# Optimization experiments

Measured on AMD Instinct MI355X. Metric: run time of the kernel, lower is better.

The kernel has to match this reference:

```python
import jax, jax.numpy as jnp
import numpy as np

N_BINS = 15


def setup_inputs() -> dict:
    key = jax.random.key(0)
    k1, k2 = jax.random.split(key)
    N, C = 500000, 100
    logits = jax.random.normal(k1, (N, C), dtype=jnp.float32)
    labels = jax.random.randint(k2, (N,), 0, C, dtype=jnp.int64)
    return {"logits": logits, "labels": labels}


def _classwise_ece(logits, labels, n_bins=N_BINS):
    # Fused equivalent of the per-class, per-bin double loop.
    # Bins are (lower, upper] with boundaries linspace(0,1,n_bins+1),
    # so bin index = ceil(p * n_bins) - 1; p == 0 falls in NO bin.
    probs = jax.nn.softmax(logits, axis=1)            # [N, C]
    N, C = probs.shape
    valid = probs > 0.0                               # p==0 matched by no (lower, upper] bin
    bin_idx = jnp.clip(jnp.ceil(probs * n_bins).astype(jnp.int32) - 1, 0, n_bins - 1)

    class_ids = jnp.arange(C, dtype=jnp.int32)[None, :]          # [1, C]
    key = (jnp.broadcast_to(class_ids * n_bins, probs.shape) + bin_idx).reshape(-1)  # [N*C]

    w = valid.astype(probs.dtype)
    correct = (labels[:, None] == class_ids).astype(probs.dtype)  # labels_in_class

    num_seg = C * n_bins
    count = jax.ops.segment_sum(w.reshape(-1), key, num_segments=num_seg).reshape(C, n_bins)
    conf_sum = jax.ops.segment_sum((probs * w).reshape(-1), key, num_segments=num_seg).reshape(C, n_bins)
    acc_sum = jax.ops.segment_sum((correct * w).reshape(-1), key, num_segments=num_seg).reshape(C, n_bins)

    # |avg_conf - acc| * prop_in_bin == |conf_sum - acc_sum| / N; empty bins give 0.
    per_class_sce = jnp.sum(jnp.abs(conf_sum - acc_sum), axis=1) / N   # [C]
    sce = jnp.mean(per_class_sce)
    return sce, per_class_sce


def reference(logits, labels):
    return _classwise_ece(logits, labels)
```

## Files before the change

### kernel.cpp

```cpp
#include <hip/hip_runtime.h>
#include <math.h>

#define NCLS 100
#define NBINS 15
#define NSEG (NCLS * NBINS)
#define NTOT (2 * NSEG + NCLS)
#define PSTRIDE 3104
#define RPI 8
#define GMAIN 2048
#define NWAVES (GMAIN * 4)

__device__ __forceinline__ void fadd(float* p, float v) { unsafeAtomicAdd(p, v); }

__device__ __forceinline__ float readlane_f(float x, int l) {
    return __builtin_bit_cast(float, __builtin_amdgcn_readlane(__builtin_bit_cast(int, x), l));
}

template <int CTRL>
__device__ __forceinline__ float dpp_add(float x) {
    int y = __builtin_amdgcn_update_dpp(0, __builtin_bit_cast(int, x),
                                        CTRL, 0xf, 0xf, true);
    return x + __builtin_bit_cast(float, y);
}


#define LOAD_TILE(E0, E1, E2, E3, LAB, TB) do {                               \
    (LAB) = labels[min((TB) + lane, N - 1)];                                  \
    const int _f = ((TB) + h) * NCLS + cqc;                                   \
    (E0) = *(const float4*)(logits + min(_f,            flim));               \
    (E1) = *(const float4*)(logits + min(_f + 2 * NCLS, flim));               \
    (E2) = *(const float4*)(logits + min(_f + 4 * NCLS, flim));               \
    (E3) = *(const float4*)(logits + min(_f + 6 * NCLS, flim));               \
} while (0)

#define EXPMASK(E, SOUT, VM) do {                                             \
    float _ex = __expf((E).x), _ey = __expf((E).y);                           \
    float _ez = __expf((E).z), _ew = __expf((E).w);                           \
    (E).x = (VM) ? _ex : 0.f; (E).y = (VM) ? _ey : 0.f;                       \
    (E).z = (VM) ? _ez : 0.f; (E).w = (VM) ? _ew : 0.f;                       \
    SOUT = ((E).x + (E).y) + ((E).z + (E).w);                                 \
} while (0)

#define CLS_TAIL(EV, J, INV, TH, LABV) do {                                   \
    t##J = fmaf((EV), (INV), t##J);                                           \
    const bool _ch = (EV) > (TH);                                             \
    const bool _lh = (cq + (J)) == (LABV);                                    \
    if (_ch || _lh) {                                                         \
        const float _p = (EV) * (INV);                                        \
        const int _b = min((int)ceilf(_p * 15.f) - 1, NBINS - 1);             \
        if (_ch) fadd(&s_conf[(cq + (J)) * NBINS + _b], _p);                  \
        if (_lh) fadd(&s_acc[(cq + (J)) * NBINS + max(_b, 0)], 1.f);          \
    }                                                                         \
} while (0)

#define SLOT_TAIL(E, K, SV, TB, LAB, FULLV, REND) do {                        \
    const float _te = readlane_f(SV, 31);                                     \
    const float _to = readlane_f(SV, 63);                                     \
    const float _S  = h ? _to : _te;                                          \
    const float _inv = __builtin_amdgcn_rcpf(fmaxf(_S, 1e-30f));              \
    const float _th  = _S * (1.0f / 15.0f);                                   \
    int _le = __builtin_amdgcn_readlane(LAB, 2 * (K));                        \
    int _lo = __builtin_amdgcn_readlane(LAB, 2 * (K) + 1);                    \
    if (!(FULLV)) {                                                           \
        if ((TB) + 2 * (K)     >= (REND)) _le = -1;                           \
        if ((TB) + 2 * (K) + 1 >= (REND)) _lo = -1;                           \
    }                                                                         \
    const int _lab = h ? _lo : _le;                                           \
    CLS_TAIL((E).x, 0, _inv, _th, _lab);                                      \
    CLS_TAIL((E).y, 1, _inv, _th, _lab);                                      \
    CLS_TAIL((E).z, 2, _inv, _th, _lab);                                      \
    CLS_TAIL((E).w, 3, _inv, _th, _lab);                                      \
} while (0)

#define COMPUTE_TILE(E0, E1, E2, E3, LAB, TB, FULLV, REND) do {               \
    const bool _v0 = act && ((FULLV) || ((TB) + 0 + h) < (REND));             \
    const bool _v1 = act && ((FULLV) || ((TB) + 2 + h) < (REND));             \
    const bool _v2 = act && ((FULLV) || ((TB) + 4 + h) < (REND));             \
    const bool _v3 = act && ((FULLV) || ((TB) + 6 + h) < (REND));             \
    float _s0, _s1, _s2, _s3;                                                 \
    EXPMASK(E0, _s0, _v0); EXPMASK(E1, _s1, _v1);                             \
    EXPMASK(E2, _s2, _v2); EXPMASK(E3, _s3, _v3);                             \
    _s0 = dpp_add<0x111>(_s0); _s1 = dpp_add<0x111>(_s1);                     \
    _s2 = dpp_add<0x111>(_s2); _s3 = dpp_add<0x111>(_s3);                     \
    _s0 = dpp_add<0x112>(_s0); _s1 = dpp_add<0x112>(_s1);                     \
    _s2 = dpp_add<0x112>(_s2); _s3 = dpp_add<0x112>(_s3);                     \
    _s0 = dpp_add<0x114>(_s0); _s1 = dpp_add<0x114>(_s1);                     \
    _s2 = dpp_add<0x114>(_s2); _s3 = dpp_add<0x114>(_s3);                     \
    _s0 = dpp_add<0x118>(_s0); _s1 = dpp_add<0x118>(_s1);                     \
    _s2 = dpp_add<0x118>(_s2); _s3 = dpp_add<0x118>(_s3);                     \
    _s0 = dpp_add<0x142>(_s0); _s1 = dpp_add<0x142>(_s1);                     \
    _s2 = dpp_add<0x142>(_s2); _s3 = dpp_add<0x142>(_s3);                     \
    SLOT_TAIL(E0, 0, _s0, TB, LAB, FULLV, REND);                              \
    SLOT_TAIL(E1, 1, _s1, TB, LAB, FULLV, REND);                              \
    SLOT_TAIL(E2, 2, _s2, TB, LAB, FULLV, REND);                              \
    SLOT_TAIL(E3, 3, _s3, TB, LAB, FULLV, REND);                              \
} while (0)

__global__ __launch_bounds__(256, 8) void ece_main_kernel(
    const float* __restrict__ logits,
    const int* __restrict__ labels,
    float* __restrict__ g_hist,
    float* __restrict__ parts,
    int N)
{
    __shared__ float s_conf[NSEG];
    __shared__ float s_acc[NSEG];
    __shared__ float s_total[NCLS];
    for (int i = threadIdx.x; i < NSEG; i += 256) { s_conf[i] = 0.f; s_acc[i] = 0.f; }
    if (threadIdx.x < NCLS) s_total[threadIdx.x] = 0.f;
    __syncthreads();

    const int lane  = threadIdx.x & 63;
    const int wave  = threadIdx.x >> 6;
    const int gwave = blockIdx.x * 4 + wave;
    const int q     = lane & 31;
    const int h     = lane >> 5;
    const int cq    = 4 * q;
    const int cqc   = min(cq, NCLS - 4);
    const bool act  = (q < NCLS / 4);
    const int flim  = N * NCLS - 4;

    const int per  = N / NWAVES;
    const int rem  = N - per * NWAVES;
    const int r0   = gwave * per + min(gwave, rem);
    const int rend = r0 + per + (gwave < rem ? 1 : 0);

    float t0 = 0.f, t1 = 0.f, t2 = 0.f, t3 = 0.f;
    float4 A0, A1, A2, A3, B0, B1, B2, B3;
    int labA, labB;
    int base = r0;

    LOAD_TILE(A0, A1, A2, A3, labA, base);
    while (base + 2 * RPI <= rend) {
        LOAD_TILE(B0, B1, B2, B3, labB, base + RPI);
        __builtin_amdgcn_sched_barrier(0);
        COMPUTE_TILE(A0, A1, A2, A3, labA, base, true, rend);
        LOAD_TILE(A0, A1, A2, A3, labA, base + 2 * RPI);
        __builtin_amdgcn_sched_barrier(0);
        COMPUTE_TILE(B0, B1, B2, B3, labB, base + RPI, true, rend);
        base += 2 * RPI;
    }
    if (base < rend)
        COMPUTE_TILE(A0, A1, A2, A3, labA, base, false, rend);
    if (base + RPI < rend) {
        LOAD_TILE(B0, B1, B2, B3, labB, base + RPI);
        COMPUTE_TILE(B0, B1, B2, B3, labB, base + RPI, false, rend);
    }

    if (act) {
        fadd(&s_total[cq + 0], t0);
        fadd(&s_total[cq + 1], t1);
        fadd(&s_total[cq + 2], t2);
        fadd(&s_total[cq + 3], t3);
    }
    __syncthreads();

    if (parts) {
        float* my = parts + (size_t)blockIdx.x * PSTRIDE;
        for (int i = threadIdx.x; i < NSEG; i += 256) {
            my[i] = s_conf[i];
            my[NSEG + i] = s_acc[i];
        }
        if (threadIdx.x < NCLS)
            my[2 * NSEG + threadIdx.x] = s_total[threadIdx.x];
    } else {
        for (int i = threadIdx.x; i < NSEG; i += 256) {
            float v = s_conf[i]; if (v != 0.f) fadd(&g_hist[i], v);
            float a = s_acc[i];  if (a != 0.f) fadd(&g_hist[NSEG + i], a);
        }
        if (threadIdx.x < NCLS) {
            float tt = s_total[threadIdx.x];
            if (tt != 0.f) fadd(&g_hist[2 * NSEG + threadIdx.x], tt);
        }
    }
}

__global__ __launch_bounds__(1024) void ece_reduce_kernel(
    const float* __restrict__ parts, float* __restrict__ g_hist, int nparts)
{
    const int lane = threadIdx.x & 63;
    const int wave = threadIdx.x >> 6;
    const int cell = blockIdx.x * 64 + lane;
    const int per = nparts / 16;
    float s = 0.f;
    if (cell < NTOT) {
        const float* bp = parts + (size_t)wave * per * PSTRIDE + cell;
        #pragma unroll 8
        for (int p = 0; p < per; ++p)
            s += bp[(size_t)p * PSTRIDE];
    }
    __shared__ float red[16][64];
    red[wave][lane] = s;
    __syncthreads();
    if (wave == 0) {
        float v = 0.f;
        #pragma unroll
        for (int w = 0; w < 16; ++w) v += red[w][lane];
        if (cell < NTOT) g_hist[cell] = v;
    }
}

__global__ __launch_bounds__(128) void ece_final_kernel(
    const float* __restrict__ g_hist,
    float* __restrict__ out,
    float invN)
{
    __shared__ float red[128];
    const int t = threadIdx.x;
    float s = 0.f;
    if (t < NCLS) {
        float conf0 = g_hist[2 * NSEG + t];
        float sum = 0.f;
        #pragma unroll
        for (int b = 1; b < NBINS; ++b) {
            float cb = g_hist[t * NBINS + b];
            float ab = g_hist[NSEG + t * NBINS + b];
            conf0 -= cb;
            sum += fabsf(cb - ab);
        }
        sum += fabsf(conf0 - g_hist[NSEG + t * NBINS + 0]);
        s = sum * invN;
        out[1 + t] = s;
    }
    red[t] = s;
    __syncthreads();
    #pragma unroll
    for (int off = 64; off > 0; off >>= 1) {
        if (t < off) red[t] += red[t + off];
        __syncthreads();
    }
    if (t == 0) out[0] = red[0] * (1.0f / (float)NCLS);
}

extern "C" void kernel_launch(void* const* d_in, const int* in_sizes, int n_in,
                              void* d_out, int out_size, void* d_ws, size_t ws_size,
                              hipStream_t stream)
{
    const float* logits = (const float*)d_in[0];
    const int*   labels = (const int*)d_in[1];
    const int N = in_sizes[1];
    float* out = (float*)d_out;

    float* g_hist = (float*)d_ws;
    const size_t parts_off = ((size_t)NTOT * sizeof(float) + 255) & ~(size_t)255;
    const size_t need = parts_off + (size_t)GMAIN * PSTRIDE * sizeof(float);
    float* parts = (ws_size >= need) ? (float*)((char*)d_ws + parts_off) : nullptr;

    if (!parts)
        (void)hipMemsetAsync(d_ws, 0, (size_t)NTOT * sizeof(float), stream);

    ece_main_kernel<<<GMAIN, 256, 0, stream>>>(logits, labels, g_hist, parts, N);
    if (parts)
        ece_reduce_kernel<<<(NTOT + 63) / 64, 1024, 0, stream>>>(parts, g_hist, GMAIN);
    ece_final_kernel<<<1, 128, 0, stream>>>(g_hist, out, 1.0f / (float)N);
}
```

Measured before the change: 347.9 us.

## Stage logits through LDS with async global_load_lds double buffering

Replaces the per-lane float4 register loads with direct global-to-LDS loads (global_load_lds). Each wave owns a double-buffered 16-row staging area, uses grid-strided tiles instead of contiguous per-wave ranges, and cuts the grid from 2048 to 512 blocks with lower occupancy bounds. The aim is fully coalesced contiguous loads that overlap with the exp/histogram compute and use fewer registers for in-flight data. In exchange it adds an LDS round trip, relies on a manual vmcnt wait count (including the label load) for correctness, and runs fewer waves to hide latency.

```diff
diff --git a/kernel.cpp b/kernel.cpp
--- a/kernel.cpp
+++ b/kernel.cpp
@@ -6,9 +6,13 @@
 #define NSEG (NCLS * NBINS)
 #define NTOT (2 * NSEG + NCLS)
 #define PSTRIDE 3104
-#define RPI 8
-#define GMAIN 2048
+#define TROWS 16
+#define GMAIN 512
 #define NWAVES (GMAIN * 4)
+#define STR (NWAVES * TROWS)
+
+#define AS1(p) ((const __attribute__((address_space(1))) void*)(p))
+#define AS3(p) ((__attribute__((address_space(3))) void*)(p))
 
 __device__ __forceinline__ void fadd(float* p, float v) { unsafeAtomicAdd(p, v); }
 
@@ -24,13 +28,17 @@
 }
 
 
-#define LOAD_TILE(E0, E1, E2, E3, LAB, TB) do {                               \
+#define STAGE(SP, TB, LAB) do {                                               \
     (LAB) = labels[min((TB) + lane, N - 1)];                                  \
-    const int _f = ((TB) + h) * NCLS + cqc;                                   \
-    (E0) = *(const float4*)(logits + min(_f,            flim));               \
-    (E1) = *(const float4*)(logits + min(_f + 2 * NCLS, flim));               \
-    (E2) = *(const float4*)(logits + min(_f + 4 * NCLS, flim));               \
-    (E3) = *(const float4*)(logits + min(_f + 6 * NCLS, flim));               \
+    const int _g = (TB) * NCLS + lane * 4;                                    \
+    __builtin_amdgcn_global_load_lds(AS1(logits + min(_g,        NC4)), AS3((SP)       ), 16, 0, 0); \
+    __builtin_amdgcn_global_load_lds(AS1(logits + min(_g +  256, NC4)), AS3((SP) + 1024), 16, 0, 0); \
+    __builtin_amdgcn_global_load_lds(AS1(logits + min(_g +  512, NC4)), AS3((SP) + 2048), 16, 0, 0); \
+    __builtin_amdgcn_global_load_lds(AS1(logits + min(_g +  768, NC4)), AS3((SP) + 3072), 16, 0, 0); \
+    __builtin_amdgcn_global_load_lds(AS1(logits + min(_g + 1024, NC4)), AS3((SP) + 4096), 16, 0, 0); \
+    __builtin_amdgcn_global_load_lds(AS1(logits + min(_g + 1280, NC4)), AS3((SP) + 5120), 16, 0, 0); \
+    const int _g1 = (TB) * NCLS + 1536 + lane;                                \
+    __builtin_amdgcn_global_load_lds(AS1(logits + min(_g1, NC1)), AS3((SP) + 6144), 4, 0, 0); \
 } while (0)
 
 #define EXPMASK(E, SOUT, VM) do {                                             \
@@ -53,17 +61,17 @@
     }                                                                         \
 } while (0)
 
-#define SLOT_TAIL(E, K, SV, TB, LAB, FULLV, REND) do {                        \
+#define SLOT_TAIL(E, J, SV, TB, LAB, FULLV) do {                              \
     const float _te = readlane_f(SV, 31);                                     \
     const float _to = readlane_f(SV, 63);                                     \
     const float _S  = h ? _to : _te;                                          \
     const float _inv = __builtin_amdgcn_rcpf(fmaxf(_S, 1e-30f));              \
     const float _th  = _S * (1.0f / 15.0f);                                   \
-    int _le = __builtin_amdgcn_readlane(LAB, 2 * (K));                        \
-    int _lo = __builtin_amdgcn_readlane(LAB, 2 * (K) + 1);                    \
+    int _le = __builtin_amdgcn_readlane(LAB, 2 * (J));                        \
+    int _lo = __builtin_amdgcn_readlane(LAB, 2 * (J) + 1);                    \
     if (!(FULLV)) {                                                           \
-        if ((TB) + 2 * (K)     >= (REND)) _le = -1;                           \
-        if ((TB) + 2 * (K) + 1 >= (REND)) _lo = -1;                           \
+        if ((TB) + 2 * (J)     >= N) _le = -1;                                \
+        if ((TB) + 2 * (J) + 1 >= N) _lo = -1;                                \
     }                                                                         \
     const int _lab = h ? _lo : _le;                                           \
     CLS_TAIL((E).x, 0, _inv, _th, _lab);                                      \
@@ -72,31 +80,59 @@
     CLS_TAIL((E).w, 3, _inv, _th, _lab);                                      \
 } while (0)
 
-#define COMPUTE_TILE(E0, E1, E2, E3, LAB, TB, FULLV, REND) do {               \
-    const bool _v0 = act && ((FULLV) || ((TB) + 0 + h) < (REND));             \
-    const bool _v1 = act && ((FULLV) || ((TB) + 2 + h) < (REND));             \
-    const bool _v2 = act && ((FULLV) || ((TB) + 4 + h) < (REND));             \
-    const bool _v3 = act && ((FULLV) || ((TB) + 6 + h) < (REND));             \
-    float _s0, _s1, _s2, _s3;                                                 \
-    EXPMASK(E0, _s0, _v0); EXPMASK(E1, _s1, _v1);                             \
-    EXPMASK(E2, _s2, _v2); EXPMASK(E3, _s3, _v3);                             \
+#define COMPUTE16(SP, TB, LAB, FULLV) do {                                    \
+    float4 F0 = *(const float4*)((SP) + ((0 + h) * 400 + cb));                \
+    float4 F1 = *(const float4*)((SP) + ((2 + h) * 400 + cb));                \
+    float4 F2 = *(const float4*)((SP) + ((4 + h) * 400 + cb));                \
+    float4 F3 = *(const float4*)((SP) + ((6 + h) * 400 + cb));                \
+    float4 F4 = *(const float4*)((SP) + ((8 + h) * 400 + cb));                \
+    float4 F5 = *(const float4*)((SP) + ((10 + h) * 400 + cb));               \
+    float4 F6 = *(const float4*)((SP) + ((12 + h) * 400 + cb));               \
+    float4 F7 = *(const float4*)((SP) + ((14 + h) * 400 + cb));               \
+    const bool _w0 = act && ((FULLV) || ((TB) + 0 + h) < N);                  \
+    const bool _w1 = act && ((FULLV) || ((TB) + 2 + h) < N);                  \
+    const bool _w2 = act && ((FULLV) || ((TB) + 4 + h) < N);                  \
+    const bool _w3 = act && ((FULLV) || ((TB) + 6 + h) < N);                  \
+    const bool _w4 = act && ((FULLV) || ((TB) + 8 + h) < N);                  \
+    const bool _w5 = act && ((FULLV) || ((TB) + 10 + h) < N);                 \
+    const bool _w6 = act && ((FULLV) || ((TB) + 12 + h) < N);                 \
+    const bool _w7 = act && ((FULLV) || ((TB) + 14 + h) < N);                 \
+    float _s0, _s1, _s2, _s3, _s4, _s5, _s6, _s7;                             \
+    EXPMASK(F0, _s0, _w0); EXPMASK(F1, _s1, _w1);                             \
+    EXPMASK(F2, _s2, _w2); EXPMASK(F3, _s3, _w3);                             \
+    EXPMASK(F4, _s4, _w4); EXPMASK(F5, _s5, _w5);                             \
+    EXPMASK(F6, _s6, _w6); EXPMASK(F7, _s7, _w7);                             \
     _s0 = dpp_add<0x111>(_s0); _s1 = dpp_add<0x111>(_s1);                     \
     _s2 = dpp_add<0x111>(_s2); _s3 = dpp_add<0x111>(_s3);                     \
+    _s4 = dpp_add<0x111>(_s4); _s5 = dpp_add<0x111>(_s5);                     \
+    _s6 = dpp_add<0x111>(_s6); _s7 = dpp_add<0x111>(_s7);                     \
     _s0 = dpp_add<0x112>(_s0); _s1 = dpp_add<0x112>(_s1);                     \
     _s2 = dpp_add<0x112>(_s2); _s3 = dpp_add<0x112>(_s3);                     \
+    _s4 = dpp_add<0x112>(_s4); _s5 = dpp_add<0x112>(_s5);                     \
+    _s6 = dpp_add<0x112>(_s6); _s7 = dpp_add<0x112>(_s7);                     \
     _s0 = dpp_add<0x114>(_s0); _s1 = dpp_add<0x114>(_s1);                     \
     _s2 = dpp_add<0x114>(_s2); _s3 = dpp_add<0x114>(_s3);                     \
+    _s4 = dpp_add<0x114>(_s4); _s5 = dpp_add<0x114>(_s5);                     \
+    _s6 = dpp_add<0x114>(_s6); _s7 = dpp_add<0x114>(_s7);                     \
     _s0 = dpp_add<0x118>(_s0); _s1 = dpp_add<0x118>(_s1);                     \
     _s2 = dpp_add<0x118>(_s2); _s3 = dpp_add<0x118>(_s3);                     \
+    _s4 = dpp_add<0x118>(_s4); _s5 = dpp_add<0x118>(_s5);                     \
+    _s6 = dpp_add<0x118>(_s6); _s7 = dpp_add<0x118>(_s7);                     \
     _s0 = dpp_add<0x142>(_s0); _s1 = dpp_add<0x142>(_s1);                     \
     _s2 = dpp_add<0x142>(_s2); _s3 = dpp_add<0x142>(_s3);                     \
-    SLOT_TAIL(E0, 0, _s0, TB, LAB, FULLV, REND);                              \
-    SLOT_TAIL(E1, 1, _s1, TB, LAB, FULLV, REND);                              \
-    SLOT_TAIL(E2, 2, _s2, TB, LAB, FULLV, REND);                              \
-    SLOT_TAIL(E3, 3, _s3, TB, LAB, FULLV, REND);                              \
-} while (0)
-
-__global__ __launch_bounds__(256, 8) void ece_main_kernel(
+    _s4 = dpp_add<0x142>(_s4); _s5 = dpp_add<0x142>(_s5);                     \
+    _s6 = dpp_add<0x142>(_s6); _s7 = dpp_add<0x142>(_s7);                     \
+    SLOT_TAIL(F0, 0, _s0, TB, LAB, FULLV);                                    \
+    SLOT_TAIL(F1, 1, _s1, TB, LAB, FULLV);                                    \
+    SLOT_TAIL(F2, 2, _s2, TB, LAB, FULLV);                                    \
+    SLOT_TAIL(F3, 3, _s3, TB, LAB, FULLV);                                    \
+    SLOT_TAIL(F4, 4, _s4, TB, LAB, FULLV);                                    \
+    SLOT_TAIL(F5, 5, _s5, TB, LAB, FULLV);                                    \
+    SLOT_TAIL(F6, 6, _s6, TB, LAB, FULLV);                                    \
+    SLOT_TAIL(F7, 7, _s7, TB, LAB, FULLV);                                    \
+} while (0)
+
+__global__ __launch_bounds__(256, 2) void ece_main_kernel(
     const float* __restrict__ logits,
     const int* __restrict__ labels,
     float* __restrict__ g_hist,
@@ -106,6 +142,7 @@
     __shared__ float s_conf[NSEG];
     __shared__ float s_acc[NSEG];
     __shared__ float s_total[NCLS];
+    __shared__ __align__(16) unsigned char s_stage[4][2][TROWS * NCLS * 4];
     for (int i = threadIdx.x; i < NSEG; i += 256) { s_conf[i] = 0.f; s_acc[i] = 0.f; }
     if (threadIdx.x < NCLS) s_total[threadIdx.x] = 0.f;
     __syncthreads();
@@ -116,35 +153,41 @@
     const int q     = lane & 31;
     const int h     = lane >> 5;
     const int cq    = 4 * q;
-    const int cqc   = min(cq, NCLS - 4);
+    const int cb    = min(cq, NCLS - 4) * 4;
     const bool act  = (q < NCLS / 4);
-    const int flim  = N * NCLS - 4;
-
-    const int per  = N / NWAVES;
-    const int rem  = N - per * NWAVES;
-    const int r0   = gwave * per + min(gwave, rem);
-    const int rend = r0 + per + (gwave < rem ? 1 : 0);
+    const int NC4   = N * NCLS - 4;
+    const int NC1   = N * NCLS - 1;
 
     float t0 = 0.f, t1 = 0.f, t2 = 0.f, t3 = 0.f;
-    float4 A0, A1, A2, A3, B0, B1, B2, B3;
-    int labA, labB;
-    int base = r0;
-
-    LOAD_TILE(A0, A1, A2, A3, labA, base);
-    while (base + 2 * RPI <= rend) {
-        LOAD_TILE(B0, B1, B2, B3, labB, base + RPI);
+    unsigned char* SP0 = &s_stage[wave][0][0];
+    unsigned char* SP1 = &s_stage[wave][1][0];
+    int labA = 0, labB = 0;
+    int base = gwave * TROWS;
+
+    if (base < N) {
+        STAGE(SP0, base, labA);
+        int nxt = base + STR;
+        bool useA = true;
+        while (nxt < N) {
+            if (useA) {
+                STAGE(SP1, nxt, labB);
+                asm volatile("s_waitcnt vmcnt(8)" ::: "memory");
+                __builtin_amdgcn_sched_barrier(0);
+                COMPUTE16(SP0, base, labA, (base + TROWS <= N));
+            } else {
+                STAGE(SP0, nxt, labA);
+                asm volatile("s_waitcnt vmcnt(8)" ::: "memory");
+                __builtin_amdgcn_sched_barrier(0);
+                COMPUTE16(SP1, base, labB, (base + TROWS <= N));
+            }
+            useA = !useA;
+            base = nxt;
+            nxt += STR;
+        }
+        asm volatile("s_waitcnt vmcnt(0)" ::: "memory");
         __builtin_amdgcn_sched_barrier(0);
-        COMPUTE_TILE(A0, A1, A2, A3, labA, base, true, rend);
-        LOAD_TILE(A0, A1, A2, A3, labA, base + 2 * RPI);
-        __builtin_amdgcn_sched_barrier(0);
-        COMPUTE_TILE(B0, B1, B2, B3, labB, base + RPI, true, rend);
-        base += 2 * RPI;
-    }
-    if (base < rend)
-        COMPUTE_TILE(A0, A1, A2, A3, labA, base, false, rend);
-    if (base + RPI < rend) {
-        LOAD_TILE(B0, B1, B2, B3, labB, base + RPI);
-        COMPUTE_TILE(B0, B1, B2, B3, labB, base + RPI, false, rend);
+        if (useA) COMPUTE16(SP0, base, labA, (base + TROWS <= N));
+        else      COMPUTE16(SP1, base, labB, (base + TROWS <= N));
     }
 
     if (act) {
```

Result: faster. 285.7 us (-17.9%).
